# Kernel optimization log

Hardware: AMD Instinct MI355X
Metric: run time of the kernel (lower is better)

Reference implementation:

```python
import jax, jax.numpy as jnp
import numpy as np

N_HEAD = 16
N_FEAT = 1024
D_K = N_FEAT // N_HEAD
B, S = 2, 2048


def setup_inputs() -> dict:
    key = jax.random.key(0)
    ks = jax.random.split(key, 13)
    s = 1.0 / np.sqrt(N_FEAT)
    return {
        "query": jax.random.normal(ks[0], (B, S, N_FEAT), jnp.float32),
        "key": jax.random.normal(ks[1], (B, S, N_FEAT), jnp.float32),
        "value": jax.random.normal(ks[2], (B, S, N_FEAT), jnp.float32),
        "mask": jax.random.randint(ks[3], (B, 1, S), 0, 2).astype(bool),
        "w_q": jax.random.uniform(ks[4], (N_FEAT, N_FEAT), jnp.float32, -s, s),
        "b_q": jax.random.uniform(ks[5], (N_FEAT,), jnp.float32, -s, s),
        "w_k": jax.random.uniform(ks[6], (N_FEAT, N_FEAT), jnp.float32, -s, s),
        "b_k": jax.random.uniform(ks[7], (N_FEAT,), jnp.float32, -s, s),
        "w_v": jax.random.uniform(ks[8], (N_FEAT, N_FEAT), jnp.float32, -s, s),
        "b_v": jax.random.uniform(ks[9], (N_FEAT,), jnp.float32, -s, s),
        "w_o": jax.random.uniform(ks[10], (N_FEAT, N_FEAT), jnp.float32, -s, s),
        "b_o": jax.random.uniform(ks[11], (N_FEAT,), jnp.float32, -s, s),
    }


def reference(query, key, value, mask, w_q, b_q, w_k, b_k, w_v, b_v, w_o, b_o):
    b = query.shape[0]
    # projections -> [b, h, s, d_k]
    def proj(x, w, bias):
        y = x @ w.T + bias
        return y.reshape(b, -1, N_HEAD, D_K).transpose(0, 2, 1, 3)

    q = proj(query, w_q, b_q)
    k = proj(key, w_k, b_k)
    v = proj(value, w_v, b_v)

    scores = jnp.einsum("bhqd,bhkd->bhqk", q, k) / jnp.sqrt(jnp.asarray(D_K, q.dtype))
    m = mask[:, None]  # [b,1,1,s] broadcast over heads and query positions
    scores = jnp.where(m, jnp.asarray(-10000.0, scores.dtype), scores)
    attn = jax.nn.softmax(scores, axis=-1)
    attn = jnp.where(m, jnp.asarray(0.0, attn.dtype), attn)
    x = jnp.einsum("bhqk,bhkd->bhqd", attn, v)
    x = x.transpose(0, 2, 1, 3).reshape(b, -1, N_HEAD * D_K)
    return x @ w_o.T + b_o
```

## Files before the change

### kernel.cpp

```cpp
#include <hip/hip_runtime.h>
#include <hip/hip_bf16.h>


typedef float f32x4 __attribute__((ext_vector_type(4)));
typedef short bf16x8 __attribute__((ext_vector_type(8)));

typedef const __attribute__((address_space(1))) void* gas_ptr;
typedef __attribute__((address_space(3))) void* las_ptr;

#if __has_builtin(__builtin_amdgcn_exp2f)
#define EXP2(x) __builtin_amdgcn_exp2f(x)
#else
#define EXP2(x) exp2f(x)
#endif
#define LOG2E 1.4426950408889634f

static __device__ __forceinline__ short to_bf16s(float f) {
    __hip_bfloat16 h = __float2bfloat16(f);
    return __builtin_bit_cast(short, h);
}
static __device__ __forceinline__ unsigned pack_bf16(float a, float b) {
    unsigned lo = (unsigned short)__builtin_bit_cast(short, __float2bfloat16(a));
    unsigned hi = (unsigned short)__builtin_bit_cast(short, __float2bfloat16(b));
    return lo | (hi << 16);
}
static __device__ __forceinline__ bf16x8 pack8(const float* p) {
    unsigned d0 = pack_bf16(p[0], p[1]);
    unsigned d1 = pack_bf16(p[2], p[3]);
    unsigned d2 = pack_bf16(p[4], p[5]);
    unsigned d3 = pack_bf16(p[6], p[7]);
    unsigned u4[4] = {d0, d1, d2, d3};
    return __builtin_bit_cast(bf16x8, u4);
}

__global__ void cvt3_kernel(const float* __restrict__ s0, const float* __restrict__ s1,
                            const float* __restrict__ s2, short* __restrict__ d0,
                            short* __restrict__ d1, short* __restrict__ d2) {
    const int g = blockIdx.x;
    const int sel = g >> 12;
    const int i = (g & 4095) * 256 + threadIdx.x;
    const float* s = sel == 0 ? s0 : (sel == 1 ? s1 : s2);
    short* d = sel == 0 ? d0 : (sel == 1 ? d1 : d2);
    float4 v = reinterpret_cast<const float4*>(s)[i];
    short4 o;
    o.x = to_bf16s(v.x); o.y = to_bf16s(v.y); o.z = to_bf16s(v.z); o.w = to_bf16s(v.w);
    reinterpret_cast<short4*>(d)[i] = o;
}
__global__ void cvt4_kernel(const float* __restrict__ s0, const float* __restrict__ s1,
                            const float* __restrict__ s2, const float* __restrict__ s3,
                            short* __restrict__ d0, short* __restrict__ d1,
                            short* __restrict__ d2, short* __restrict__ d3) {
    const int g = blockIdx.x;
    const int sel = g >> 10;
    const int i = (g & 1023) * 256 + threadIdx.x;
    const float* s = sel == 0 ? s0 : (sel == 1 ? s1 : (sel == 2 ? s2 : s3));
    short* d = sel == 0 ? d0 : (sel == 1 ? d1 : (sel == 2 ? d2 : d3));
    float4 v = reinterpret_cast<const float4*>(s)[i];
    short4 o;
    o.x = to_bf16s(v.x); o.y = to_bf16s(v.y); o.z = to_bf16s(v.z); o.w = to_bf16s(v.w);
    reinterpret_cast<short4*>(d)[i] = o;
}

__global__ void maskf_kernel(const int* __restrict__ mask, float* __restrict__ mf) {
    const int i = blockIdx.x * 256 + threadIdx.x;
    const int p = i & 31;
    const int phi = 8 * ((p >> 2) & 3) + 4 * (p >> 4) + (p & 3);
    mf[i] = mask[(i & ~31) | phi] ? (-10000.0f * LOG2E) : 0.0f;
}

static __device__ __forceinline__ void stage_tile(
    short* sa, short* sb, const short* A, const short* W,
    int m0, int n0, int k0, int tid)
{
#pragma unroll
    for (int rnd = 0; rnd < 2; ++rnd) {
        const int t = rnd * 256 + tid;
        const int c2 = t & 7;
        const int row = 2 * (t >> 3) + (c2 & 1);
        const int col = (c2 >> 1) * 8;
        __builtin_amdgcn_global_load_lds((gas_ptr)(A + (long)(m0 + row) * 1024 + k0 + col),
                                         (las_ptr)(sa + t * 8), 16, 0, 0);
        __builtin_amdgcn_global_load_lds((gas_ptr)(W + (long)(n0 + row) * 1024 + k0 + col),
                                         (las_ptr)(sb + t * 8), 16, 0, 0);
    }
}

static __device__ __forceinline__ void gemm_compute(
    const short* sa, const short* sb, int wr, int wc, int aoff, f32x4 (&acc)[4][4])
{
    bf16x8 af[4], bfr[4];
#pragma unroll
    for (int i = 0; i < 4; ++i)
        af[i] = *reinterpret_cast<const bf16x8*>(sa + (wr + i * 16) * 32 + aoff);
#pragma unroll
    for (int j = 0; j < 4; ++j)
        bfr[j] = *reinterpret_cast<const bf16x8*>(sb + (wc + j * 16) * 32 + aoff);
#pragma unroll
    for (int i = 0; i < 4; ++i)
#pragma unroll
        for (int j = 0; j < 4; ++j)
            acc[i][j] = __builtin_amdgcn_mfma_f32_16x16x32_bf16(af[i], bfr[j], acc[i][j], 0, 0, 0);
}

__global__ __launch_bounds__(256, 3) void proj_gemm(
    const short* __restrict__ A0, const short* __restrict__ A1, const short* __restrict__ A2,
    const short* __restrict__ W0, const short* __restrict__ W1, const short* __restrict__ W2,
    const float* __restrict__ bi0, const float* __restrict__ bi1, const float* __restrict__ bi2,
    short* __restrict__ o0, short* __restrict__ o1, short* __restrict__ o2)
{
    __shared__ __align__(16) short sa[2][4096];
    __shared__ __align__(16) short sb[2][4096];
    const int z = blockIdx.z;
    const short* A = z == 0 ? A0 : (z == 1 ? A1 : A2);
    const short* W = z == 0 ? W0 : (z == 1 ? W1 : W2);
    const float* bias = z == 0 ? bi0 : (z == 1 ? bi1 : bi2);
    short* outp = z == 0 ? o0 : (z == 1 ? o1 : o2);

    const int tid = threadIdx.x;
    const int w = tid >> 6, l = tid & 63;
    const int lr = l & 15, lh = l >> 4;
    const int m0 = blockIdx.x * 128, n0 = blockIdx.y * 128;
    const int wr = (w >> 1) * 64, wc = (w & 1) * 64;
    const int aoff = (lr >> 1) * 64 + (lr & 1) * 8 + lh * 16;

    f32x4 acc[4][4] = {};

    stage_tile(sa[0], sb[0], A, W, m0, n0, 0, tid);
    __syncthreads();
    for (int k0 = 0; k0 < 1024; k0 += 64) {
        stage_tile(sa[1], sb[1], A, W, m0, n0, k0 + 32, tid);
        gemm_compute(sa[0], sb[0], wr, wc, aoff, acc);
        __syncthreads();
        if (k0 + 64 < 1024)
            stage_tile(sa[0], sb[0], A, W, m0, n0, k0 + 64, tid);
        gemm_compute(sa[1], sb[1], wr, wc, aoff, acc);
        __syncthreads();
    }

    const float scl = (z == 0) ? 0.125f * LOG2E : 1.0f;
#pragma unroll
    for (int i = 0; i < 4; ++i) {
#pragma unroll
        for (int j = 0; j < 4; ++j) {
#pragma unroll
            for (int r = 0; r < 4; ++r) {
                const int row = m0 + wr + i * 16 + lh * 4 + r;
                const int col = n0 + wc + j * 16 + lr;
                const float v = (acc[i][j][r] + bias[col]) * scl;
                const int b = row >> 11, s = row & 2047;
                const int h = col >> 6, d = col & 63;
                if (z != 2)
                    outp[(((long)(b * 16 + h)) * 2048 + s) * 64 + d] = to_bf16s(v);
                else
                    outp[(((long)(b * 16 + h)) * 64 + d) * 2048 + s] = to_bf16s(v);
            }
        }
    }
}

__global__ __launch_bounds__(256, 2) void out_gemm(
    const short* __restrict__ A, const short* __restrict__ W,
    const float* __restrict__ bias, float* __restrict__ outp)
{
    __shared__ __align__(16) short sa[2][4096];
    __shared__ __align__(16) short sb[2][2048];
    const int tid = threadIdx.x;
    const int w = tid >> 6, l = tid & 63;
    const int lr = l & 15, lh = l >> 4;
    const int m0 = blockIdx.x * 128, n0 = blockIdx.y * 64;
    const int wr = (w >> 1) * 64, wc = (w & 1) * 32;
    const int aoff = (lr >> 1) * 64 + (lr & 1) * 8 + lh * 16;

    f32x4 acc[4][2] = {};

    const int c2 = tid & 7;
    const int brow = 2 * (tid >> 3) + (c2 & 1);
    const int bcol = (c2 >> 1) * 8;

    auto stage = [&](short* pa, short* pb, int k0) {
#pragma unroll
        for (int rnd = 0; rnd < 2; ++rnd) {
            const int t = rnd * 256 + tid;
            const int cc = t & 7;
            const int row = 2 * (t >> 3) + (cc & 1);
            const int col = (cc >> 1) * 8;
            __builtin_amdgcn_global_load_lds((gas_ptr)(A + (long)(m0 + row) * 1024 + k0 + col),
                                             (las_ptr)(pa + t * 8), 16, 0, 0);
        }
        __builtin_amdgcn_global_load_lds((gas_ptr)(W + (long)(n0 + brow) * 1024 + k0 + bcol),
                                         (las_ptr)(pb + tid * 8), 16, 0, 0);
    };
    auto compute = [&](const short* pa, const short* pb) {
        bf16x8 af[4], bfr[2];
#pragma unroll
        for (int i = 0; i < 4; ++i)
            af[i] = *reinterpret_cast<const bf16x8*>(pa + (wr + i * 16) * 32 + aoff);
#pragma unroll
        for (int j = 0; j < 2; ++j)
            bfr[j] = *reinterpret_cast<const bf16x8*>(pb + (wc + j * 16) * 32 + aoff);
#pragma unroll
        for (int i = 0; i < 4; ++i)
#pragma unroll
            for (int j = 0; j < 2; ++j)
                acc[i][j] = __builtin_amdgcn_mfma_f32_16x16x32_bf16(af[i], bfr[j], acc[i][j], 0, 0, 0);
    };

    stage(sa[0], sb[0], 0);
    __syncthreads();
    for (int k0 = 0; k0 < 1024; k0 += 64) {
        stage(sa[1], sb[1], k0 + 32);
        compute(sa[0], sb[0]);
        __syncthreads();
        if (k0 + 64 < 1024)
            stage(sa[0], sb[0], k0 + 64);
        compute(sa[1], sb[1]);
        __syncthreads();
    }

#pragma unroll
    for (int i = 0; i < 4; ++i)
#pragma unroll
        for (int j = 0; j < 2; ++j)
#pragma unroll
            for (int r = 0; r < 4; ++r) {
                const int row = m0 + wr + i * 16 + lh * 4 + r;
                const int col = n0 + wc + j * 16 + lr;
                outp[(long)row * 1024 + col] = acc[i][j][r] + bias[col];
            }
}


static __device__ __forceinline__ void stage_kv(
    short* ldsKb, short* ldsVb, const short* Kg, const short* Vg,
    int key0, int w, int srow, int prow, int schunk)
{
    __builtin_amdgcn_global_load_lds((gas_ptr)(Kg + (long)(key0 + prow) * 64 + schunk * 8),
                                     (las_ptr)(ldsKb + w * 512), 16, 0, 0);
    __builtin_amdgcn_global_load_lds((gas_ptr)(Kg + (long)(key0 + 32 + prow) * 64 + schunk * 8),
                                     (las_ptr)(ldsKb + 2048 + w * 512), 16, 0, 0);
    __builtin_amdgcn_global_load_lds((gas_ptr)(Vg + (long)srow * 2048 + key0 + schunk * 8),
                                     (las_ptr)(ldsVb + w * 512), 16, 0, 0);
    __builtin_amdgcn_global_load_lds((gas_ptr)(Vg + (long)(srow + 32) * 2048 + key0 + schunk * 8),
                                     (las_ptr)(ldsVb + 2048 + w * 512), 16, 0, 0);
}

static __device__ __forceinline__ void attn_step(
    const short* __restrict__ Kbuf, const short* __restrict__ Vbuf,
    const float* __restrict__ ldsM, int key0,
    const bf16x8 (&qf)[2][2], int lr, int lh, int sw,
    float (&mreg)[2], float (&lsum)[2], f32x4 (&ao)[2][4])
{
    f32x4 mb[4];
#pragma unroll
    for (int s = 0; s < 4; ++s)
        mb[s] = *reinterpret_cast<const f32x4*>(ldsM + key0 + s * 16 + lh * 4);

    f32x4 sc[2][4];
#pragma unroll
    for (int s = 0; s < 4; ++s) {
        const short* kb = Kbuf + (s * 16 + lr) * 64;
        bf16x8 k0 = *reinterpret_cast<const bf16x8*>(kb + (((lh * 16) ^ sw) >> 1));
        bf16x8 k1 = *reinterpret_cast<const bf16x8*>(kb + (((64 + lh * 16) ^ sw) >> 1));
        sc[0][s] = __builtin_amdgcn_mfma_f32_16x16x32_bf16(k0, qf[0][0], mb[s], 0, 0, 0);
        sc[0][s] = __builtin_amdgcn_mfma_f32_16x16x32_bf16(k1, qf[0][1], sc[0][s], 0, 0, 0);
        sc[1][s] = __builtin_amdgcn_mfma_f32_16x16x32_bf16(k0, qf[1][0], mb[s], 0, 0, 0);
        sc[1][s] = __builtin_amdgcn_mfma_f32_16x16x32_bf16(k1, qf[1][1], sc[1][s], 0, 0, 0);
    }

    bf16x8 pb[2][2];
#pragma unroll
    for (int j = 0; j < 2; ++j) {
        float m0 = fmaxf(fmaxf(fmaxf(sc[j][0][0], sc[j][0][1]), sc[j][0][2]), sc[j][0][3]);
        float m1 = fmaxf(fmaxf(fmaxf(sc[j][1][0], sc[j][1][1]), sc[j][1][2]), sc[j][1][3]);
        float m2 = fmaxf(fmaxf(fmaxf(sc[j][2][0], sc[j][2][1]), sc[j][2][2]), sc[j][2][3]);
        float m3 = fmaxf(fmaxf(fmaxf(sc[j][3][0], sc[j][3][1]), sc[j][3][2]), sc[j][3][3]);
        float t = fmaxf(fmaxf(m0, m1), fmaxf(m2, m3));
        t = fmaxf(t, __shfl_xor(t, 16));
        t = fmaxf(t, __shfl_xor(t, 32));
        if (__any(t > mreg[j] + 8.0f)) {
            const float mn = fmaxf(mreg[j], t);
            const float sf = EXP2(mreg[j] - mn);
            lsum[j] *= sf;
#pragma unroll
            for (int d4 = 0; d4 < 4; ++d4) ao[j][d4] *= sf;
            mreg[j] = mn;
        }
        float p[16], ps = 0.f;
#pragma unroll
        for (int s = 0; s < 4; ++s) {
#pragma unroll
            for (int r = 0; r < 4; ++r) {
                const float e = EXP2(sc[j][s][r] - mreg[j]);
                p[s * 4 + r] = e;
                ps += e;
            }
        }
        ps += __shfl_xor(ps, 16);
        ps += __shfl_xor(ps, 32);
        lsum[j] += ps;
        pb[j][0] = pack8(p);
        pb[j][1] = pack8(p + 8);
    }

#pragma unroll
    for (int c = 0; c < 2; ++c) {
#pragma unroll
        for (int d4 = 0; d4 < 4; ++d4) {
            const short* vb = Vbuf + (d4 * 16 + lr) * 64;
            bf16x8 vf = *reinterpret_cast<const bf16x8*>(vb + (((c * 64 + lh * 16) ^ sw) >> 1));
            ao[0][d4] = __builtin_amdgcn_mfma_f32_16x16x32_bf16(vf, pb[0][c], ao[0][d4], 0, 0, 0);
            ao[1][d4] = __builtin_amdgcn_mfma_f32_16x16x32_bf16(vf, pb[1][c], ao[1][d4], 0, 0, 0);
        }
    }
}

__global__ __launch_bounds__(256, 2) void attn_kernel(
    const short* __restrict__ Q, const short* __restrict__ Kmat,
    const short* __restrict__ Vt, const float* __restrict__ maskf,
    short* __restrict__ X)
{
    __shared__ __align__(16) short ldsK[2][4096];
    __shared__ __align__(16) short ldsV[2][4096];
    __shared__ __align__(16) float ldsM[2048];

    const int id = blockIdx.x;
    const int slot = id >> 3;
    const int bh = (id & 7) * 4 + (slot >> 4);
    const int q0 = (slot & 15) * 128;
    const int b = bh >> 4, h = bh & 15;
    const int w = threadIdx.x >> 6, l = threadIdx.x & 63;
    const int lr = l & 15, lh = l >> 4;
    const int sw = (lr & 7) << 4;

    const int srow = w * 8 + (l >> 3);
    const int schunk = (l & 7) ^ (srow & 7);
    const int prow = 8 * ((srow >> 2) & 3) + 4 * (srow >> 4) + (srow & 3);

    const short* Kg = Kmat + (long)bh * 2048 * 64;
    const short* Vg = Vt + (long)bh * 64 * 2048;

#pragma unroll
    for (int rnd = 0; rnd < 2; ++rnd) {
        const int t = rnd * 256 + threadIdx.x;
        __builtin_amdgcn_global_load_lds((gas_ptr)(maskf + (long)b * 2048 + t * 4),
                                         (las_ptr)(ldsM + t * 4), 16, 0, 0);
    }

    const short* Qp = Q + ((long)bh * 2048 + q0 + w * 32 + lr) * 64 + lh * 8;
    bf16x8 qf[2][2];
    qf[0][0] = *reinterpret_cast<const bf16x8*>(Qp);
    qf[0][1] = *reinterpret_cast<const bf16x8*>(Qp + 32);
    qf[1][0] = *reinterpret_cast<const bf16x8*>(Qp + 16 * 64);
    qf[1][1] = *reinterpret_cast<const bf16x8*>(Qp + 16 * 64 + 32);

    float mreg[2] = {-1e30f, -1e30f}, lsum[2] = {0.f, 0.f};
    f32x4 ao[2][4] = {};

    stage_kv(ldsK[0], ldsV[0], Kg, Vg, 0, w, srow, prow, schunk);
    __syncthreads();

    for (int tt = 0; tt < 16; ++tt) {
        const int key0 = tt * 128;
        stage_kv(ldsK[1], ldsV[1], Kg, Vg, key0 + 64, w, srow, prow, schunk);
        attn_step(ldsK[0], ldsV[0], ldsM, key0, qf, lr, lh, sw, mreg, lsum, ao);
        __syncthreads();
        if (tt < 15)
            stage_kv(ldsK[0], ldsV[0], Kg, Vg, key0 + 128, w, srow, prow, schunk);
        attn_step(ldsK[1], ldsV[1], ldsM, key0 + 64, qf, lr, lh, sw, mreg, lsum, ao);
        __syncthreads();
    }

#pragma unroll
    for (int j = 0; j < 2; ++j) {
        const float inv = 1.0f / fmaxf(lsum[j], 1e-30f);
        const int s = q0 + w * 32 + j * 16 + lr;
        short* Xp = X + ((long)b * 2048 + s) * 1024 + h * 64 + lh * 4;
#pragma unroll
        for (int d4 = 0; d4 < 4; ++d4) {
            short4 o;
            o.x = to_bf16s(ao[j][d4][0] * inv);
            o.y = to_bf16s(ao[j][d4][1] * inv);
            o.z = to_bf16s(ao[j][d4][2] * inv);
            o.w = to_bf16s(ao[j][d4][3] * inv);
            *reinterpret_cast<short4*>(Xp + d4 * 16) = o;
        }
    }
}

extern "C" void kernel_launch(void* const* d_in, const int* in_sizes, int n_in,
                              void* d_out, int out_size, void* d_ws, size_t ws_size,
                              hipStream_t stream) {
    const float* query = (const float*)d_in[0];
    const float* key_  = (const float*)d_in[1];
    const float* value = (const float*)d_in[2];
    const int*   mask  = (const int*)d_in[3];
    const float* w_q = (const float*)d_in[4];
    const float* b_q = (const float*)d_in[5];
    const float* w_k = (const float*)d_in[6];
    const float* b_k = (const float*)d_in[7];
    const float* w_v = (const float*)d_in[8];
    const float* b_v = (const float*)d_in[9];
    const float* w_o = (const float*)d_in[10];
    const float* b_o = (const float*)d_in[11];

    const long SEQ = 4194304;
    const long WSZ = 1048576;
    short* ws = (short*)d_ws;
    short* cq = ws;
    short* ck = cq + SEQ;
    short* cv = ck + SEQ;
    short* wq = cv + SEQ;
    short* wk = wq + WSZ;
    short* wv = wk + WSZ;
    short* wo = wv + WSZ;
    short* Qb = wo + WSZ;
    short* Kb = Qb + SEQ;
    short* Vt = Kb + SEQ;
    short* Xb = cq;
    float* mkf = (float*)cv;

    cvt3_kernel<<<12288, 256, 0, stream>>>(query, key_, value, cq, ck, cv);
    cvt4_kernel<<<4096, 256, 0, stream>>>(w_q, w_k, w_v, w_o, wq, wk, wv, wo);

    dim3 blk(256);
    proj_gemm<<<dim3(32, 8, 3), blk, 0, stream>>>(cq, ck, cv, wq, wk, wv,
                                                  b_q, b_k, b_v, Qb, Kb, Vt);

    maskf_kernel<<<16, 256, 0, stream>>>(mask, mkf);

    attn_kernel<<<512, blk, 0, stream>>>(Qb, Kb, Vt, mkf, Xb);

    out_gemm<<<dim3(32, 16), blk, 0, stream>>>(Xb, wo, b_o, (float*)d_out);
}
```

Baseline: 146.8 us.

## Halve attention query tile per block, double grid, and use packed bf16 conversion

Each attention block now covers 64 query rows instead of 128, with each wave owning 16 rows, so the grid doubles to 1024 blocks and launch bounds allow 4 blocks per CU. Register state per wave drops, which is meant to raise occupancy and keep the CUs busier. The cost is that every K/V tile is staged into LDS twice as often across the grid, which halves the reuse of each loaded tile. Probability packing and output conversion also switch to the hardware v_cvt_pk_bf16_f32 instruction via inline asm.

```diff
diff --git a/kernel.cpp b/kernel.cpp
--- a/kernel.cpp
+++ b/kernel.cpp
@@ -19,18 +19,10 @@
     __hip_bfloat16 h = __float2bfloat16(f);
     return __builtin_bit_cast(short, h);
 }
-static __device__ __forceinline__ unsigned pack_bf16(float a, float b) {
-    unsigned lo = (unsigned short)__builtin_bit_cast(short, __float2bfloat16(a));
-    unsigned hi = (unsigned short)__builtin_bit_cast(short, __float2bfloat16(b));
-    return lo | (hi << 16);
-}
-static __device__ __forceinline__ bf16x8 pack8(const float* p) {
-    unsigned d0 = pack_bf16(p[0], p[1]);
-    unsigned d1 = pack_bf16(p[2], p[3]);
-    unsigned d2 = pack_bf16(p[4], p[5]);
-    unsigned d3 = pack_bf16(p[6], p[7]);
-    unsigned u4[4] = {d0, d1, d2, d3};
-    return __builtin_bit_cast(bf16x8, u4);
+static __device__ __forceinline__ unsigned cvtpk(float lo, float hi) {
+    unsigned r;
+    asm("v_cvt_pk_bf16_f32 %0, %1, %2" : "=v"(r) : "v"(lo), "v"(hi));
+    return r;
 }
 
 __global__ void cvt3_kernel(const float* __restrict__ s0, const float* __restrict__ s1,
@@ -247,74 +239,72 @@
 static __device__ __forceinline__ void attn_step(
     const short* __restrict__ Kbuf, const short* __restrict__ Vbuf,
     const float* __restrict__ ldsM, int key0,
-    const bf16x8 (&qf)[2][2], int lr, int lh, int sw,
-    float (&mreg)[2], float (&lsum)[2], f32x4 (&ao)[2][4])
+    const bf16x8 qf0, const bf16x8 qf1, int lr, int lh, int sw,
+    float& mreg, float& lsum, f32x4 (&ao)[4])
 {
     f32x4 mb[4];
 #pragma unroll
     for (int s = 0; s < 4; ++s)
         mb[s] = *reinterpret_cast<const f32x4*>(ldsM + key0 + s * 16 + lh * 4);
 
-    f32x4 sc[2][4];
+    f32x4 sc[4];
 #pragma unroll
     for (int s = 0; s < 4; ++s) {
         const short* kb = Kbuf + (s * 16 + lr) * 64;
         bf16x8 k0 = *reinterpret_cast<const bf16x8*>(kb + (((lh * 16) ^ sw) >> 1));
         bf16x8 k1 = *reinterpret_cast<const bf16x8*>(kb + (((64 + lh * 16) ^ sw) >> 1));
-        sc[0][s] = __builtin_amdgcn_mfma_f32_16x16x32_bf16(k0, qf[0][0], mb[s], 0, 0, 0);
-        sc[0][s] = __builtin_amdgcn_mfma_f32_16x16x32_bf16(k1, qf[0][1], sc[0][s], 0, 0, 0);
-        sc[1][s] = __builtin_amdgcn_mfma_f32_16x16x32_bf16(k0, qf[1][0], mb[s], 0, 0, 0);
-        sc[1][s] = __builtin_amdgcn_mfma_f32_16x16x32_bf16(k1, qf[1][1], sc[1][s], 0, 0, 0);
-    }
-
-    bf16x8 pb[2][2];
-#pragma unroll
-    for (int j = 0; j < 2; ++j) {
-        float m0 = fmaxf(fmaxf(fmaxf(sc[j][0][0], sc[j][0][1]), sc[j][0][2]), sc[j][0][3]);
-        float m1 = fmaxf(fmaxf(fmaxf(sc[j][1][0], sc[j][1][1]), sc[j][1][2]), sc[j][1][3]);
-        float m2 = fmaxf(fmaxf(fmaxf(sc[j][2][0], sc[j][2][1]), sc[j][2][2]), sc[j][2][3]);
-        float m3 = fmaxf(fmaxf(fmaxf(sc[j][3][0], sc[j][3][1]), sc[j][3][2]), sc[j][3][3]);
-        float t = fmaxf(fmaxf(m0, m1), fmaxf(m2, m3));
-        t = fmaxf(t, __shfl_xor(t, 16));
-        t = fmaxf(t, __shfl_xor(t, 32));
-        if (__any(t > mreg[j] + 8.0f)) {
-            const float mn = fmaxf(mreg[j], t);
-            const float sf = EXP2(mreg[j] - mn);
-            lsum[j] *= sf;
-#pragma unroll
-            for (int d4 = 0; d4 < 4; ++d4) ao[j][d4] *= sf;
-            mreg[j] = mn;
+        sc[s] = __builtin_amdgcn_mfma_f32_16x16x32_bf16(k0, qf0, mb[s], 0, 0, 0);
+        sc[s] = __builtin_amdgcn_mfma_f32_16x16x32_bf16(k1, qf1, sc[s], 0, 0, 0);
+    }
+
+    float m0 = fmaxf(fmaxf(fmaxf(sc[0][0], sc[0][1]), sc[0][2]), sc[0][3]);
+    float m1 = fmaxf(fmaxf(fmaxf(sc[1][0], sc[1][1]), sc[1][2]), sc[1][3]);
+    float m2 = fmaxf(fmaxf(fmaxf(sc[2][0], sc[2][1]), sc[2][2]), sc[2][3]);
+    float m3 = fmaxf(fmaxf(fmaxf(sc[3][0], sc[3][1]), sc[3][2]), sc[3][3]);
+    float t = fmaxf(fmaxf(m0, m1), fmaxf(m2, m3));
+    t = fmaxf(t, __shfl_xor(t, 16));
+    t = fmaxf(t, __shfl_xor(t, 32));
+    if (__any(t > mreg + 8.0f)) {
+        const float mn = fmaxf(mreg, t);
+        const float sf = EXP2(mreg - mn);
+        lsum *= sf;
+#pragma unroll
+        for (int d4 = 0; d4 < 4; ++d4) ao[d4] *= sf;
+        mreg = mn;
+    }
+    float p[16], ps = 0.f;
+#pragma unroll
+    for (int s = 0; s < 4; ++s) {
+#pragma unroll
+        for (int r = 0; r < 4; ++r) {
+            const float e = EXP2(sc[s][r] - mreg);
+            p[s * 4 + r] = e;
+            ps += e;
         }
-        float p[16], ps = 0.f;
-#pragma unroll
-        for (int s = 0; s < 4; ++s) {
-#pragma unroll
-            for (int r = 0; r < 4; ++r) {
-                const float e = EXP2(sc[j][s][r] - mreg[j]);
-                p[s * 4 + r] = e;
-                ps += e;
-            }
-        }
-        ps += __shfl_xor(ps, 16);
-        ps += __shfl_xor(ps, 32);
-        lsum[j] += ps;
-        pb[j][0] = pack8(p);
-        pb[j][1] = pack8(p + 8);
-    }
+    }
+    ps += __shfl_xor(ps, 16);
+    ps += __shfl_xor(ps, 32);
+    lsum += ps;
+
+    unsigned pw[8];
+#pragma unroll
+    for (int i = 0; i < 8; ++i) pw[i] = cvtpk(p[2 * i], p[2 * i + 1]);
+    const bf16x8 pb0 = __builtin_bit_cast(bf16x8, *(ulonglong2*)&pw[0]);
+    const bf16x8 pb1 = __builtin_bit_cast(bf16x8, *(ulonglong2*)&pw[4]);
 
 #pragma unroll
     for (int c = 0; c < 2; ++c) {
+        const bf16x8 pbc = c == 0 ? pb0 : pb1;
 #pragma unroll
         for (int d4 = 0; d4 < 4; ++d4) {
             const short* vb = Vbuf + (d4 * 16 + lr) * 64;
             bf16x8 vf = *reinterpret_cast<const bf16x8*>(vb + (((c * 64 + lh * 16) ^ sw) >> 1));
-            ao[0][d4] = __builtin_amdgcn_mfma_f32_16x16x32_bf16(vf, pb[0][c], ao[0][d4], 0, 0, 0);
-            ao[1][d4] = __builtin_amdgcn_mfma_f32_16x16x32_bf16(vf, pb[1][c], ao[1][d4], 0, 0, 0);
+            ao[d4] = __builtin_amdgcn_mfma_f32_16x16x32_bf16(vf, pbc, ao[d4], 0, 0, 0);
         }
     }
 }
 
-__global__ __launch_bounds__(256, 2) void attn_kernel(
+__global__ __launch_bounds__(256, 4) void attn_kernel(
     const short* __restrict__ Q, const short* __restrict__ Kmat,
     const short* __restrict__ Vt, const float* __restrict__ maskf,
     short* __restrict__ X)
@@ -325,8 +315,8 @@
 
     const int id = blockIdx.x;
     const int slot = id >> 3;
-    const int bh = (id & 7) * 4 + (slot >> 4);
-    const int q0 = (slot & 15) * 128;
+    const int bh = (id & 7) * 4 + (slot >> 5);
+    const int q0 = (slot & 31) * 64;
     const int b = bh >> 4, h = bh & 15;
     const int w = threadIdx.x >> 6, l = threadIdx.x & 63;
     const int lr = l & 15, lh = l >> 4;
@@ -346,15 +336,12 @@
                                          (las_ptr)(ldsM + t * 4), 16, 0, 0);
     }
 
-    const short* Qp = Q + ((long)bh * 2048 + q0 + w * 32 + lr) * 64 + lh * 8;
-    bf16x8 qf[2][2];
-    qf[0][0] = *reinterpret_cast<const bf16x8*>(Qp);
-    qf[0][1] = *reinterpret_cast<const bf16x8*>(Qp + 32);
-    qf[1][0] = *reinterpret_cast<const bf16x8*>(Qp + 16 * 64);
-    qf[1][1] = *reinterpret_cast<const bf16x8*>(Qp + 16 * 64 + 32);
-
-    float mreg[2] = {-1e30f, -1e30f}, lsum[2] = {0.f, 0.f};
-    f32x4 ao[2][4] = {};
+    const short* Qp = Q + ((long)bh * 2048 + q0 + w * 16 + lr) * 64 + lh * 8;
+    const bf16x8 qf0 = *reinterpret_cast<const bf16x8*>(Qp);
+    const bf16x8 qf1 = *reinterpret_cast<const bf16x8*>(Qp + 32);
+
+    float mreg = -1e30f, lsum = 0.f;
+    f32x4 ao[4] = {};
 
     stage_kv(ldsK[0], ldsV[0], Kg, Vg, 0, w, srow, prow, schunk);
     __syncthreads();
@@ -362,28 +349,23 @@
     for (int tt = 0; tt < 16; ++tt) {
         const int key0 = tt * 128;
         stage_kv(ldsK[1], ldsV[1], Kg, Vg, key0 + 64, w, srow, prow, schunk);
-        attn_step(ldsK[0], ldsV[0], ldsM, key0, qf, lr, lh, sw, mreg, lsum, ao);
+        attn_step(ldsK[0], ldsV[0], ldsM, key0, qf0, qf1, lr, lh, sw, mreg, lsum, ao);
         __syncthreads();
         if (tt < 15)
             stage_kv(ldsK[0], ldsV[0], Kg, Vg, key0 + 128, w, srow, prow, schunk);
-        attn_step(ldsK[1], ldsV[1], ldsM, key0 + 64, qf, lr, lh, sw, mreg, lsum, ao);
-        __syncthreads();
-    }
-
-#pragma unroll
-    for (int j = 0; j < 2; ++j) {
-        const float inv = 1.0f / fmaxf(lsum[j], 1e-30f);
-        const int s = q0 + w * 32 + j * 16 + lr;
-        short* Xp = X + ((long)b * 2048 + s) * 1024 + h * 64 + lh * 4;
-#pragma unroll
-        for (int d4 = 0; d4 < 4; ++d4) {
-            short4 o;
-            o.x = to_bf16s(ao[j][d4][0] * inv);
-            o.y = to_bf16s(ao[j][d4][1] * inv);
-            o.z = to_bf16s(ao[j][d4][2] * inv);
-            o.w = to_bf16s(ao[j][d4][3] * inv);
-            *reinterpret_cast<short4*>(Xp + d4 * 16) = o;
-        }
+        attn_step(ldsK[1], ldsV[1], ldsM, key0 + 64, qf0, qf1, lr, lh, sw, mreg, lsum, ao);
+        __syncthreads();
+    }
+
+    const float inv = 1.0f / fmaxf(lsum, 1e-30f);
+    const int s = q0 + w * 16 + lr;
+    short* Xp = X + ((long)b * 2048 + s) * 1024 + h * 64 + lh * 4;
+#pragma unroll
+    for (int d4 = 0; d4 < 4; ++d4) {
+        uint2 o;
+        o.x = cvtpk(ao[d4][0] * inv, ao[d4][1] * inv);
+        o.y = cvtpk(ao[d4][2] * inv, ao[d4][3] * inv);
+        *reinterpret_cast<uint2*>(Xp + d4 * 16) = o;
     }
 }
 
@@ -428,7 +410,7 @@
 
     maskf_kernel<<<16, 256, 0, stream>>>(mask, mkf);
 
-    attn_kernel<<<512, blk, 0, stream>>>(Qb, Kb, Vt, mkf, Xb);
+    attn_kernel<<<1024, blk, 0, stream>>>(Qb, Kb, Vt, mkf, Xb);
 
     out_gemm<<<dim3(32, 16), blk, 0, stream>>>(Xb, wo, b_o, (float*)d_out);
 }
```

Measured after the change: 142.3 us. 1.03x faster.
